# Kernel optimization log

Hardware: AMD Instinct MI355X
Metric: run time of the kernel (lower is better)

Reference implementation:

```python
import jax, jax.numpy as jnp
import numpy as np

N, B, C, K, H = 65536, 4, 512, 256, 8


def setup_inputs() -> dict:
    key = jax.random.key(0)
    ks = jax.random.split(key, 6)
    feat = jax.random.normal(ks[0], (N, C), dtype=jnp.float32)
    cls_tokens = jax.random.normal(ks[1], (B, C), dtype=jnp.float32)
    Wqkv = jax.random.normal(ks[2], (C, 3 * C), dtype=jnp.float32) * 0.02
    bqkv = jnp.zeros((3 * C,), dtype=jnp.float32)
    Wproj = jax.random.normal(ks[3], (C, C), dtype=jnp.float32) * 0.02
    bproj = jnp.zeros((C,), dtype=jnp.float32)
    order = jax.random.permutation(ks[4], N)          # serialized order (permutation)
    inverse = jnp.argsort(order)                       # its inverse
    offset = jnp.arange(1, B + 1) * (N // B)           # equal-size point clouds, divisible by K
    return {"feat": feat, "cls_tokens": cls_tokens, "Wqkv": Wqkv, "bqkv": bqkv,
            "Wproj": Wproj, "bproj": bproj, "order": order, "inverse": inverse,
            "offset": offset, "patch_size": K, "num_heads": H}


def reference(feat, cls_tokens, Wqkv, bqkv, Wproj, bproj, order, inverse, offset, patch_size, num_heads):
    n, c = feat.shape
    b = offset.shape[0]
    k = patch_size
    h = num_heads
    dh = c // h
    scale = dh ** -0.5
    n_chunks = n // k

    # qkv projection, gather into serialized order
    qkv = (feat @ Wqkv + bqkv)[order]                  # [N, 3C]
    cls_qkv = cls_tokens @ Wqkv + bqkv                 # [B, 3C]

    # chunk -> batch assignment (offsets are chunk-aligned here)
    chunk_starts = jnp.arange(n_chunks) * k
    batch_id = jnp.searchsorted(offset, chunk_starts, side="right")  # [n_chunks]
    acc = jax.nn.one_hot(batch_id, b, dtype=feat.dtype)              # [n_chunks, B]
    agg = acc.T / acc.T.sum(axis=1, keepdims=True)                   # [B, n_chunks]

    cls_per_chunk = acc @ cls_qkv                                    # [n_chunks, 3C]
    qkv_c = qkv.reshape(n_chunks, k, 3 * c)
    qkv_c = jnp.concatenate([cls_per_chunk[:, None, :], qkv_c], axis=1)  # [n_chunks, K+1, 3C]

    qkv_c = qkv_c.reshape(n_chunks, k + 1, 3, h, dh)
    q = qkv_c[:, :, 0].transpose(0, 2, 1, 3)           # [n_chunks, H, K+1, dh]
    kk = qkv_c[:, :, 1].transpose(0, 2, 1, 3)
    v = qkv_c[:, :, 2].transpose(0, 2, 1, 3)

    # upcast_attention / upcast_softmax = True
    attn = jnp.einsum("nhqd,nhkd->nhqk", q.astype(jnp.float32) * scale, kk.astype(jnp.float32))
    attn = jax.nn.softmax(attn, axis=-1).astype(feat.dtype)
    out = jnp.einsum("nhqk,nhkd->nhqd", attn, v)       # [n_chunks, H, K+1, dh]
    out = out.transpose(0, 2, 1, 3).reshape(n_chunks, k + 1, c)

    feat_out = out[:, 1:, :].reshape(-1, c)[inverse]   # scatter back to original order
    feat_out = feat_out @ Wproj + bproj                # proj (proj_drop is identity in eval)
    cls_feat = agg @ out[:, 0, :]                      # [B, C] (no proj, per source)
    return feat_out, cls_feat
```

## Files before the change

kernel.cpp:

```cpp
#include <hip/hip_runtime.h>


typedef float  floatx4 __attribute__((ext_vector_type(4)));
typedef __bf16 bf16x8  __attribute__((ext_vector_type(8)));

__device__ __forceinline__ __bf16 f2bf(float x) {
  unsigned u = __builtin_bit_cast(unsigned, x);
  u = u + 0x7FFFu + ((u >> 16) & 1u);
  unsigned short h = (unsigned short)(u >> 16);
  return __builtin_bit_cast(__bf16, h);
}

__device__ __forceinline__ floatx4 mfma_16x16x32(bf16x8 a, bf16x8 b, floatx4 c) {
  return __builtin_amdgcn_mfma_f32_16x16x32_bf16(a, b, c, 0, 0, 0);
}

__device__ __forceinline__ void gload16(const void* g, void* l) {
  __builtin_amdgcn_global_load_lds(
      (const __attribute__((address_space(1))) unsigned int*)g,
      (__attribute__((address_space(3))) unsigned int*)l, 16, 0, 0);
}

__global__ void cast_gather_feat(const float* __restrict__ feat,
                                 const int* __restrict__ order,
                                 __bf16* __restrict__ dst) {
  long i = ((long)blockIdx.x * blockDim.x + threadIdx.x) * 8;
  int row = (int)(i >> 9);
  int col = (int)(i & 511);
  const float* sp = feat + (long)order[row] * 512 + col;
  float4 a = *(const float4*)sp;
  float4 b = *(const float4*)(sp + 4);
  bf16x8 o;
  o[0] = f2bf(a.x); o[1] = f2bf(a.y); o[2] = f2bf(a.z); o[3] = f2bf(a.w);
  o[4] = f2bf(b.x); o[5] = f2bf(b.y); o[6] = f2bf(b.z); o[7] = f2bf(b.w);
  *(bf16x8*)(dst + i) = o;
}

__global__ void cast_wT(const float* __restrict__ W, __bf16* __restrict__ Wt,
                        int K, int N, int total) {
  int i = blockIdx.x * blockDim.x + threadIdx.x;
  if (i >= total) return;
  int n = i / K, k = i - n * K;
  Wt[i] = f2bf(W[(long)k * N + n]);
}

__global__ void cls_qkv_kernel(const float* __restrict__ cls_tokens,
                               const float* __restrict__ Wqkv,
                               const float* __restrict__ bqkv,
                               __bf16* __restrict__ clsqkv, int Bn, int C, int N3) {
  int i = blockIdx.x * blockDim.x + threadIdx.x;
  if (i >= Bn * N3) return;
  int b = i / N3, n = i - b * N3;
  float sv = bqkv[n];
  for (int k = 0; k < C; ++k) sv += cls_tokens[b * C + k] * Wqkv[(long)k * N3 + n];
  clsqkv[i] = f2bf(sv);
}

template <int OUT_F32>
__global__ __launch_bounds__(256, 2) void gemm_bt(
    const __bf16* __restrict__ A, const __bf16* __restrict__ Bt,
    const float* __restrict__ bias, void* __restrict__ C,
    int N, int K) {
  __shared__ __align__(16) __bf16 As[128 * 64];
  __shared__ __align__(16) __bf16 Bs[128 * 64];
  const int tid = threadIdx.x;
  const int wave = tid >> 6, lane = tid & 63;
  const int quad = lane >> 4, l15 = lane & 15;
  const int wr = wave >> 1, wc = wave & 1;
  const long m0 = (long)blockIdx.x * 128;
  const int n0 = blockIdx.y * 128;
  const int srow8 = lane >> 3;
  const int sc8p = lane & 7;

  floatx4 zero = {0.f, 0.f, 0.f, 0.f};
  floatx4 acc[4][4];
#pragma unroll
  for (int i = 0; i < 4; ++i)
#pragma unroll
    for (int j = 0; j < 4; ++j) acc[i][j] = zero;

  for (int kt = 0; kt < K; kt += 64) {
    __syncthreads();
#pragma unroll
    for (int i = 0; i < 4; ++i) {
      const int rbase = i * 32 + wave * 8;
      const int row = rbase + srow8;
      const int c8 = sc8p ^ (row & 7);
      gload16(A + (m0 + row) * K + kt + c8 * 8, As + rbase * 64);
      gload16(Bt + (long)(n0 + row) * K + kt + c8 * 8, Bs + rbase * 64);
    }
    __syncthreads();
#pragma unroll
    for (int ks = 0; ks < 2; ++ks) {
      bf16x8 af[4], bfr[4];
#pragma unroll
      for (int mi = 0; mi < 4; ++mi) {
        int row = wr * 64 + mi * 16 + l15;
        int c8 = ks * 4 + quad;
        af[mi] = *(const bf16x8*)(As + row * 64 + ((c8 ^ (row & 7)) << 3));
      }
#pragma unroll
      for (int ni = 0; ni < 4; ++ni) {
        int row = wc * 64 + ni * 16 + l15;
        int c8 = ks * 4 + quad;
        bfr[ni] = *(const bf16x8*)(Bs + row * 64 + ((c8 ^ (row & 7)) << 3));
      }
#pragma unroll
      for (int mi = 0; mi < 4; ++mi)
#pragma unroll
        for (int ni = 0; ni < 4; ++ni)
          acc[mi][ni] = mfma_16x16x32(af[mi], bfr[ni], acc[mi][ni]);
    }
  }
#pragma unroll
  for (int mi = 0; mi < 4; ++mi) {
#pragma unroll
    for (int ni = 0; ni < 4; ++ni) {
      const int col = n0 + wc * 64 + ni * 16 + l15;
      const float bb = bias[col];
#pragma unroll
      for (int r = 0; r < 4; ++r) {
        const long row = m0 + wr * 64 + mi * 16 + quad * 4 + r;
        float v = acc[mi][ni][r] + bb;
        if (OUT_F32)
          ((float*)C)[row * N + col] = v;
        else
          ((__bf16*)C)[row * N + col] = f2bf(v);
      }
    }
  }
}

__global__ __launch_bounds__(256, 2) void attn_kernel(
    const __bf16* __restrict__ qkv,
    const __bf16* __restrict__ clsqkv,
    const int* __restrict__ order,
    const int* __restrict__ offset,
    __bf16* __restrict__ outO,
    float* __restrict__ outcls,
    int B) {
  __shared__ __align__(16) __bf16 Vt[64 * 296];
  __shared__ __align__(16) __bf16 Pbuf[4 * 16 * 40];
  const int chunk = blockIdx.x >> 3;
  const int h = blockIdx.x & 7;
  const int tid = threadIdx.x;
  const int wave = tid >> 6, lane = tid & 63;
  const int quad = lane >> 4, l15 = lane & 15;
  const int cs = chunk << 8;
  int batch = 0;
  for (int b = 0; b < B; ++b) batch += (offset[b] <= cs) ? 1 : 0;
  const __bf16* clsrow = clsqkv + (long)batch * 1536;
  const int qoff = h * 64;
  const int koff = 512 + h * 64;
  const int voff = 1024 + h * 64;

  {
    int t = tid;
    const __bf16* rp = (t == 0) ? clsrow : (qkv + (long)(cs + t - 1) * 1536);
#pragma unroll
    for (int i = 0; i < 8; ++i) {
      bf16x8 v = *(const bf16x8*)(rp + voff + i * 8);
#pragma unroll
      for (int j = 0; j < 8; ++j) Vt[(i * 8 + j) * 296 + t] = v[j];
    }
  }
  if (tid < 32) {
    int t = 256 + tid;
    if (t == 256) {
      const __bf16* rp = qkv + (long)(cs + 255) * 1536;
#pragma unroll
      for (int i = 0; i < 8; ++i) {
        bf16x8 v = *(const bf16x8*)(rp + voff + i * 8);
#pragma unroll
        for (int j = 0; j < 8; ++j) Vt[(i * 8 + j) * 296 + t] = v[j];
      }
    } else {
      const __bf16 z = f2bf(0.f);
      for (int d = 0; d < 64; ++d) Vt[d * 296 + t] = z;
    }
  }
  __syncthreads();

  __bf16* Pw = Pbuf + wave * 640;

  for (int rt = wave; rt < 17; rt += 4) {
    int qtok = rt * 16 + l15;
    const __bf16* qp = (qtok == 0) ? clsrow
                       : (qkv + (long)(cs + ((qtok <= 256) ? qtok : 256) - 1) * 1536);
    bf16x8 qf0 = *(const bf16x8*)(qp + qoff + quad * 8);
    bf16x8 qf1 = *(const bf16x8*)(qp + qoff + 32 + quad * 8);

    floatx4 zero = {0.f, 0.f, 0.f, 0.f};
    floatx4 s[18];
#pragma unroll
    for (int i = 0; i < 18; ++i) s[i] = zero;
#pragma unroll
    for (int kt2 = 0; kt2 < 18; ++kt2) {
      int ktok = kt2 * 16 + l15;
      const __bf16* kp = (ktok == 0) ? clsrow
                         : (qkv + (long)(cs + ((ktok <= 256) ? ktok : 256) - 1) * 1536);
      bf16x8 kf0 = *(const bf16x8*)(kp + koff + quad * 8);
      bf16x8 kf1 = *(const bf16x8*)(kp + koff + 32 + quad * 8);
      s[kt2] = mfma_16x16x32(qf0, kf0, s[kt2]);
      s[kt2] = mfma_16x16x32(qf1, kf1, s[kt2]);
    }
    float mx[4] = {-3.0e38f, -3.0e38f, -3.0e38f, -3.0e38f};
#pragma unroll
    for (int kt2 = 0; kt2 < 18; ++kt2) {
      const bool valid = (kt2 * 16 + l15) < 257;
#pragma unroll
      for (int r = 0; r < 4; ++r) {
        float v = s[kt2][r] * 0.125f;
        v = valid ? v : -3.0e38f;
        s[kt2][r] = v;
        mx[r] = fmaxf(mx[r], v);
      }
    }
#pragma unroll
    for (int off = 1; off < 16; off <<= 1)
#pragma unroll
      for (int r = 0; r < 4; ++r) mx[r] = fmaxf(mx[r], __shfl_xor(mx[r], off, 16));
    float sum[4] = {0.f, 0.f, 0.f, 0.f};
#pragma unroll
    for (int kt2 = 0; kt2 < 18; ++kt2)
#pragma unroll
      for (int r = 0; r < 4; ++r) {
        float e = __expf(s[kt2][r] - mx[r]);
        s[kt2][r] = e;
        sum[r] += e;
      }
#pragma unroll
    for (int off = 1; off < 16; off <<= 1)
#pragma unroll
      for (int r = 0; r < 4; ++r) sum[r] += __shfl_xor(sum[r], off, 16);
    float rl[4];
#pragma unroll
    for (int r = 0; r < 4; ++r) rl[r] = 1.0f / sum[r];

    floatx4 o[4];
#pragma unroll
    for (int i = 0; i < 4; ++i) o[i] = zero;
#pragma unroll
    for (int ks = 0; ks < 9; ++ks) {
#pragma unroll
      for (int half = 0; half < 2; ++half) {
        int kt2 = ks * 2 + half;
#pragma unroll
        for (int r = 0; r < 4; ++r)
          Pw[(quad * 4 + r) * 40 + half * 16 + l15] = f2bf(s[kt2][r] * rl[r]);
      }
      asm volatile("s_waitcnt lgkmcnt(0)" ::: "memory");
      bf16x8 pf = *(const bf16x8*)(Pw + l15 * 40 + quad * 8);
#pragma unroll
      for (int ni = 0; ni < 4; ++ni) {
        bf16x8 vf = *(const bf16x8*)(Vt + (ni * 16 + l15) * 296 + ks * 32 + quad * 8);
        o[ni] = mfma_16x16x32(pf, vf, o[ni]);
      }
    }
#pragma unroll
    for (int r = 0; r < 4; ++r) {
      int q = rt * 16 + quad * 4 + r;
      if (q > 256) continue;
      if (q == 0) {
#pragma unroll
        for (int ni = 0; ni < 4; ++ni)
          outcls[(long)chunk * 512 + h * 64 + ni * 16 + l15] = o[ni][r];
      } else {
        long orow = (long)order[cs + q - 1];
#pragma unroll
        for (int ni = 0; ni < 4; ++ni)
          outO[orow * 512 + h * 64 + ni * 16 + l15] = f2bf(o[ni][r]);
      }
    }
  }
}

__global__ void cls_feat_kernel(const float* __restrict__ outcls,
                                const int* __restrict__ offset,
                                float* __restrict__ dst, int B, int C) {
  int i = blockIdx.x * blockDim.x + threadIdx.x;
  if (i >= B * C) return;
  int b = i / C, c = i - b * C;
  int st = (b == 0) ? 0 : offset[b - 1];
  int en = offset[b];
  int c0 = st >> 8, c1 = en >> 8;
  float s = 0.f;
  for (int ch = c0; ch < c1; ++ch) s += outcls[(long)ch * C + c];
  dst[i] = s / (float)(c1 - c0);
}

extern "C" void kernel_launch(void* const* d_in, const int* in_sizes, int n_in,
                              void* d_out, int out_size, void* d_ws, size_t ws_size,
                              hipStream_t stream) {
  const float* feat       = (const float*)d_in[0];
  const float* cls_tokens = (const float*)d_in[1];
  const float* Wqkv       = (const float*)d_in[2];
  const float* bqkv       = (const float*)d_in[3];
  const float* Wproj      = (const float*)d_in[4];
  const float* bproj      = (const float*)d_in[5];
  const int*   order      = (const int*)d_in[6];
  const int*   offset     = (const int*)d_in[8];
  const int B = in_sizes[8];

  char* ws = (char*)d_ws;
  __bf16* qkv    = (__bf16*)(ws);
  __bf16* featb  = (__bf16*)(ws + 201326592);
  __bf16* outO   = featb;
  __bf16* wqkvT  = (__bf16*)(ws + 268435456);
  __bf16* wprojT = (__bf16*)(ws + 270008320);
  __bf16* clsqkv = (__bf16*)(ws + 270532608);
  float*  outcls = (float*)(ws + 270544896);

  float* feat_out = (float*)d_out;
  float* cls_out  = feat_out + (long)65536 * 512;

  cast_gather_feat<<<16384, 256, 0, stream>>>(feat, order, featb);
  cast_wT<<<3072, 256, 0, stream>>>(Wqkv, wqkvT, 512, 1536, 512 * 1536);
  cast_wT<<<1024, 256, 0, stream>>>(Wproj, wprojT, 512, 512, 512 * 512);
  cls_qkv_kernel<<<24, 256, 0, stream>>>(cls_tokens, Wqkv, bqkv, clsqkv, B, 512, 1536);

  gemm_bt<0><<<dim3(512, 12), 256, 0, stream>>>(featb, wqkvT, bqkv, (void*)qkv, 1536, 512);

  attn_kernel<<<2048, 256, 0, stream>>>(qkv, clsqkv, order, offset, outO, outcls, B);

  gemm_bt<1><<<dim3(512, 4), 256, 0, stream>>>(outO, wprojT, bproj, (void*)feat_out, 512, 512);

  cls_feat_kernel<<<8, 256, 0, stream>>>(outcls, offset, cls_out, B, 512);
}
```

Measured before the change: 737.3 us.

## Tile weight transposes, split cls projection, and streamline attention softmax and indexing

Replaces the strided weight cast with a shared-memory tiled transpose and splits the cls QKV reduction across four thread groups. The attention kernel now precomputes row byte offsets in an LDS table, drops the padded 18th key tile, handles the last key token with a scalar correction, and uses exp2 with a folded scale. It also defers softmax normalisation to the output, remaps block order so heads are outer, and raises launch bounds to four blocks per SIMD. This trades more register pressure and extra shuffles for fewer MFMAs, fewer global address computations and better occupancy.

New measurement: 688.8 us. 1.07x faster.

```diff
diff --git a/kernel.cpp b/kernel.cpp
--- a/kernel.cpp
+++ b/kernel.cpp
@@ -36,24 +36,40 @@
   *(bf16x8*)(dst + i) = o;
 }
 
-__global__ void cast_wT(const float* __restrict__ W, __bf16* __restrict__ Wt,
-                        int K, int N, int total) {
-  int i = blockIdx.x * blockDim.x + threadIdx.x;
-  if (i >= total) return;
-  int n = i / K, k = i - n * K;
-  Wt[i] = f2bf(W[(long)k * N + n]);
+__global__ void transpose_cast(const float* __restrict__ W, __bf16* __restrict__ Wt,
+                               int K, int N) {
+  __shared__ float tile[32][33];
+  const int n0 = blockIdx.x * 32, k0 = blockIdx.y * 32;
+  const int c = threadIdx.x & 31, r8 = threadIdx.x >> 5;
+#pragma unroll
+  for (int i = 0; i < 4; ++i) {
+    int r = r8 + i * 8;
+    tile[r][c] = W[(long)(k0 + r) * N + n0 + c];
+  }
+  __syncthreads();
+#pragma unroll
+  for (int i = 0; i < 4; ++i) {
+    int r = r8 + i * 8;
+    Wt[(long)(n0 + r) * K + k0 + c] = f2bf(tile[c][r]);
+  }
 }
 
 __global__ void cls_qkv_kernel(const float* __restrict__ cls_tokens,
                                const float* __restrict__ Wqkv,
                                const float* __restrict__ bqkv,
-                               __bf16* __restrict__ clsqkv, int Bn, int C, int N3) {
-  int i = blockIdx.x * blockDim.x + threadIdx.x;
-  if (i >= Bn * N3) return;
-  int b = i / N3, n = i - b * N3;
-  float sv = bqkv[n];
-  for (int k = 0; k < C; ++k) sv += cls_tokens[b * C + k] * Wqkv[(long)k * N3 + n];
-  clsqkv[i] = f2bf(sv);
+                               __bf16* __restrict__ clsqkv, int N3) {
+  __shared__ float red[256];
+  const int c = threadIdx.x & 63, part = threadIdx.x >> 6;
+  const int o = blockIdx.x * 64 + c;
+  const int b = o / N3, n = o - b * N3;
+  float sv = 0.f;
+  const int kst = part * 128;
+  for (int k = kst; k < kst + 128; ++k)
+    sv += cls_tokens[b * 512 + k] * Wqkv[(long)k * N3 + n];
+  red[threadIdx.x] = sv;
+  __syncthreads();
+  if (part == 0)
+    clsqkv[o] = f2bf(red[c] + red[c + 64] + red[c + 128] + red[c + 192] + bqkv[n]);
 }
 
 template <int OUT_F32>
@@ -131,7 +147,7 @@
   }
 }
 
-__global__ __launch_bounds__(256, 2) void attn_kernel(
+__global__ __launch_bounds__(256, 4) void attn_kernel(
     const __bf16* __restrict__ qkv,
     const __bf16* __restrict__ clsqkv,
     const int* __restrict__ order,
@@ -139,94 +155,94 @@
     __bf16* __restrict__ outO,
     float* __restrict__ outcls,
     int B) {
-  __shared__ __align__(16) __bf16 Vt[64 * 296];
+  __shared__ __align__(16) __bf16 Vt[64 * 264];
   __shared__ __align__(16) __bf16 Pbuf[4 * 16 * 40];
-  const int chunk = blockIdx.x >> 3;
-  const int h = blockIdx.x & 7;
+  __shared__ unsigned ktab[272];
+  const int chunk = blockIdx.x & 255;
+  const int h = blockIdx.x >> 8;
   const int tid = threadIdx.x;
   const int wave = tid >> 6, lane = tid & 63;
   const int quad = lane >> 4, l15 = lane & 15;
   const int cs = chunk << 8;
   int batch = 0;
   for (int b = 0; b < B; ++b) batch += (offset[b] <= cs) ? 1 : 0;
-  const __bf16* clsrow = clsqkv + (long)batch * 1536;
-  const int qoff = h * 64;
-  const int koff = 512 + h * 64;
-  const int voff = 1024 + h * 64;
+  const unsigned clsoff =
+      (unsigned)((const char*)(clsqkv + (long)batch * 1536) - (const char*)qkv);
+
+  for (int t = tid; t < 272; t += 256)
+    ktab[t] = (t == 0) ? clsoff : (unsigned)(cs + ((t <= 256) ? t : 256) - 1) * 3072u;
+
+  const int qoffB = h * 128;
+  const int koffB = 1024 + h * 128;
+  const int voffB = 2048 + h * 128;
 
   {
-    int t = tid;
-    const __bf16* rp = (t == 0) ? clsrow : (qkv + (long)(cs + t - 1) * 1536);
-#pragma unroll
-    for (int i = 0; i < 8; ++i) {
-      bf16x8 v = *(const bf16x8*)(rp + voff + i * 8);
-#pragma unroll
-      for (int j = 0; j < 8; ++j) Vt[(i * 8 + j) * 296 + t] = v[j];
-    }
-  }
-  if (tid < 32) {
-    int t = 256 + tid;
-    if (t == 256) {
-      const __bf16* rp = qkv + (long)(cs + 255) * 1536;
-#pragma unroll
-      for (int i = 0; i < 8; ++i) {
-        bf16x8 v = *(const bf16x8*)(rp + voff + i * 8);
-#pragma unroll
-        for (int j = 0; j < 8; ++j) Vt[(i * 8 + j) * 296 + t] = v[j];
-      }
-    } else {
-      const __bf16 z = f2bf(0.f);
-      for (int d = 0; d < 64; ++d) Vt[d * 296 + t] = z;
+    const int rsub = lane >> 3, c8 = lane & 7;
+#pragma unroll
+    for (int p = 0; p < 8; ++p) {
+      int t = p * 32 + wave * 8 + rsub;
+      unsigned ro = (t == 0) ? clsoff : (unsigned)(cs + t - 1) * 3072u;
+      bf16x8 v = *(const bf16x8*)((const char*)qkv + ro + voffB + c8 * 16);
+#pragma unroll
+      for (int j = 0; j < 8; ++j) Vt[(c8 * 8 + j) * 264 + t] = v[j];
+    }
+    if (tid < 8) {
+      bf16x8 v = *(const bf16x8*)((const char*)qkv +
+                                  (unsigned)(cs + 255) * 3072u + voffB + tid * 16);
+#pragma unroll
+      for (int j = 0; j < 8; ++j) Vt[(tid * 8 + j) * 264 + 256] = v[j];
     }
   }
   __syncthreads();
 
-  __bf16* Pw = Pbuf + wave * 640;
+  float v256[4];
+#pragma unroll
+  for (int ni = 0; ni < 4; ++ni) v256[ni] = (float)Vt[(ni * 16 + l15) * 264 + 256];
+  __bf16* Pw = Pbuf + wave * (16 * 40);
 
   for (int rt = wave; rt < 17; rt += 4) {
-    int qtok = rt * 16 + l15;
-    const __bf16* qp = (qtok == 0) ? clsrow
-                       : (qkv + (long)(cs + ((qtok <= 256) ? qtok : 256) - 1) * 1536);
-    bf16x8 qf0 = *(const bf16x8*)(qp + qoff + quad * 8);
-    bf16x8 qf1 = *(const bf16x8*)(qp + qoff + 32 + quad * 8);
+    const unsigned qo = ktab[rt * 16 + l15];
+    bf16x8 qf0 = *(const bf16x8*)((const char*)qkv + qo + qoffB + quad * 16);
+    bf16x8 qf1 = *(const bf16x8*)((const char*)qkv + qo + qoffB + 64 + quad * 16);
 
     floatx4 zero = {0.f, 0.f, 0.f, 0.f};
-    floatx4 s[18];
-#pragma unroll
-    for (int i = 0; i < 18; ++i) s[i] = zero;
-#pragma unroll
-    for (int kt2 = 0; kt2 < 18; ++kt2) {
-      int ktok = kt2 * 16 + l15;
-      const __bf16* kp = (ktok == 0) ? clsrow
-                         : (qkv + (long)(cs + ((ktok <= 256) ? ktok : 256) - 1) * 1536);
-      bf16x8 kf0 = *(const bf16x8*)(kp + koff + quad * 8);
-      bf16x8 kf1 = *(const bf16x8*)(kp + koff + 32 + quad * 8);
-      s[kt2] = mfma_16x16x32(qf0, kf0, s[kt2]);
-      s[kt2] = mfma_16x16x32(qf1, kf1, s[kt2]);
-    }
+    floatx4 s[17];
+#pragma unroll
+    for (int i = 0; i < 17; ++i) s[i] = zero;
+#pragma unroll
+    for (int k2 = 0; k2 < 17; ++k2) {
+      const unsigned ko = ktab[k2 * 16 + l15];
+      bf16x8 kf0 = *(const bf16x8*)((const char*)qkv + ko + koffB + quad * 16);
+      bf16x8 kf1 = *(const bf16x8*)((const char*)qkv + ko + koffB + 64 + quad * 16);
+      s[k2] = mfma_16x16x32(qf0, kf0, s[k2]);
+      s[k2] = mfma_16x16x32(qf1, kf1, s[k2]);
+    }
+
     float mx[4] = {-3.0e38f, -3.0e38f, -3.0e38f, -3.0e38f};
 #pragma unroll
-    for (int kt2 = 0; kt2 < 18; ++kt2) {
-      const bool valid = (kt2 * 16 + l15) < 257;
+    for (int k2 = 0; k2 < 16; ++k2)
+#pragma unroll
+      for (int r = 0; r < 4; ++r) mx[r] = fmaxf(mx[r], s[k2][r]);
+#pragma unroll
+    for (int r = 0; r < 4; ++r) {
+      float v = (l15 == 0) ? s[16][r] : -3.0e38f;
+      s[16][r] = v;
+      mx[r] = fmaxf(mx[r], v);
+    }
+#pragma unroll
+    for (int off = 1; off < 16; off <<= 1)
+#pragma unroll
+      for (int r = 0; r < 4; ++r) mx[r] = fmaxf(mx[r], __shfl_xor(mx[r], off, 16));
+    const float c1 = 0.125f * 1.44269504f;
+    float mb[4], sum[4] = {0.f, 0.f, 0.f, 0.f};
+#pragma unroll
+    for (int r = 0; r < 4; ++r) mb[r] = mx[r] * c1;
+#pragma unroll
+    for (int k2 = 0; k2 < 17; ++k2)
 #pragma unroll
       for (int r = 0; r < 4; ++r) {
-        float v = s[kt2][r] * 0.125f;
-        v = valid ? v : -3.0e38f;
-        s[kt2][r] = v;
-        mx[r] = fmaxf(mx[r], v);
-      }
-    }
-#pragma unroll
-    for (int off = 1; off < 16; off <<= 1)
-#pragma unroll
-      for (int r = 0; r < 4; ++r) mx[r] = fmaxf(mx[r], __shfl_xor(mx[r], off, 16));
-    float sum[4] = {0.f, 0.f, 0.f, 0.f};
-#pragma unroll
-    for (int kt2 = 0; kt2 < 18; ++kt2)
-#pragma unroll
-      for (int r = 0; r < 4; ++r) {
-        float e = __expf(s[kt2][r] - mx[r]);
-        s[kt2][r] = e;
+        float e = __builtin_amdgcn_exp2f(fmaf(s[k2][r], c1, -mb[r]));
+        s[k2][r] = e;
         sum[r] += e;
       }
 #pragma unroll
@@ -241,22 +257,31 @@
 #pragma unroll
     for (int i = 0; i < 4; ++i) o[i] = zero;
 #pragma unroll
-    for (int ks = 0; ks < 9; ++ks) {
+    for (int ks = 0; ks < 8; ++ks) {
 #pragma unroll
       for (int half = 0; half < 2; ++half) {
         int kt2 = ks * 2 + half;
 #pragma unroll
         for (int r = 0; r < 4; ++r)
-          Pw[(quad * 4 + r) * 40 + half * 16 + l15] = f2bf(s[kt2][r] * rl[r]);
+          Pw[(quad * 4 + r) * 40 + half * 16 + l15] = f2bf(s[kt2][r]);
       }
       asm volatile("s_waitcnt lgkmcnt(0)" ::: "memory");
       bf16x8 pf = *(const bf16x8*)(Pw + l15 * 40 + quad * 8);
 #pragma unroll
       for (int ni = 0; ni < 4; ++ni) {
-        bf16x8 vf = *(const bf16x8*)(Vt + (ni * 16 + l15) * 296 + ks * 32 + quad * 8);
+        bf16x8 vf = *(const bf16x8*)(Vt + (ni * 16 + l15) * 264 + ks * 32 + quad * 8);
         o[ni] = mfma_16x16x32(pf, vf, o[ni]);
       }
     }
+    float p256[4];
+#pragma unroll
+    for (int r = 0; r < 4; ++r) p256[r] = __shfl(s[16][r], lane & 48, 64);
+#pragma unroll
+    for (int ni = 0; ni < 4; ++ni)
+#pragma unroll
+      for (int r = 0; r < 4; ++r)
+        o[ni][r] = (o[ni][r] + p256[r] * v256[ni]) * rl[r];
+
 #pragma unroll
     for (int r = 0; r < 4; ++r) {
       int q = rt * 16 + quad * 4 + r;
@@ -315,9 +340,9 @@
   float* cls_out  = feat_out + (long)65536 * 512;
 
   cast_gather_feat<<<16384, 256, 0, stream>>>(feat, order, featb);
-  cast_wT<<<3072, 256, 0, stream>>>(Wqkv, wqkvT, 512, 1536, 512 * 1536);
-  cast_wT<<<1024, 256, 0, stream>>>(Wproj, wprojT, 512, 512, 512 * 512);
-  cls_qkv_kernel<<<24, 256, 0, stream>>>(cls_tokens, Wqkv, bqkv, clsqkv, B, 512, 1536);
+  transpose_cast<<<dim3(48, 16), 256, 0, stream>>>(Wqkv, wqkvT, 512, 1536);
+  transpose_cast<<<dim3(16, 16), 256, 0, stream>>>(Wproj, wprojT, 512, 512);
+  cls_qkv_kernel<<<96, 256, 0, stream>>>(cls_tokens, Wqkv, bqkv, clsqkv, 1536);
 
   gemm_bt<0><<<dim3(512, 12), 256, 0, stream>>>(featb, wqkvT, bqkv, (void*)qkv, 1536, 512);
 
```
